# Performance work log

Measured on AMD Instinct MI355X. Metric: run time of the kernel, lower is better.

The kernel has to match this reference:

```python
import jax, jax.numpy as jnp
import numpy as np

N_NODES = 50000
N_EDGES = 600000
N_GRAPHS = 64
IN_DIM = 6
HID = 128


def setup_inputs() -> dict:
    key = jax.random.key(0)
    ks = jax.random.split(key, 10)
    x = jax.random.normal(ks[0], (N_NODES, IN_DIM), dtype=jnp.float32)
    edge_index = jax.random.randint(ks[1], (2, N_EDGES), 0, N_NODES, dtype=jnp.int64)
    batch = jnp.sort(jax.random.randint(ks[2], (N_NODES,), 0, N_GRAPHS, dtype=jnp.int64))
    def glorot(k, shape):
        lim = float(np.sqrt(6.0 / (shape[0] + shape[1])))
        return jax.random.uniform(k, shape, jnp.float32, -lim, lim)
    return {
        'x': x, 'edge_index': edge_index, 'batch': batch,
        'W1': glorot(ks[3], (IN_DIM, HID)), 'b1': jnp.zeros((HID,), jnp.float32),
        'W2': glorot(ks[4], (HID, HID)), 'b2': jnp.zeros((HID,), jnp.float32),
        'W3': glorot(ks[5], (HID, HID)), 'b3': jnp.zeros((HID,), jnp.float32),
        'fc1_w': glorot(ks[6], (HID, 64)), 'fc1_b': jnp.zeros((64,), jnp.float32),
        'fc2_w': glorot(ks[7], (64, 1)), 'fc2_b': jnp.zeros((1,), jnp.float32),
    }


def _gcn_norm(edge_index, n):
    # PyG GCNConv default: add self-loops, symmetric D^-1/2 A D^-1/2 normalization.
    loop = jnp.arange(n, dtype=edge_index.dtype)
    src = jnp.concatenate([edge_index[0], loop])
    dst = jnp.concatenate([edge_index[1], loop])
    deg = jax.ops.segment_sum(jnp.ones_like(dst, dtype=jnp.float32), dst, num_segments=n)
    dis = jnp.where(deg > 0, jax.lax.rsqrt(jnp.maximum(deg, 1.0)), 0.0)
    norm = dis[src] * dis[dst]  # [E+N]
    return src, dst, norm


def _gcn_layer(x, W, b, src, dst, norm, n):
    h = x @ W                       # [N, H] small GEMM
    msg = h[src] * norm[:, None]    # [E+N, H] irregular gather
    out = jax.ops.segment_sum(msg, dst, num_segments=n)  # scatter-add
    return out + b


def reference(x, edge_index, batch, W1, b1, W2, b2, W3, b3, fc1_w, fc1_b, fc2_w, fc2_b):
    n = x.shape[0]
    src, dst, norm = _gcn_norm(edge_index, n)
    h = jax.nn.relu(_gcn_layer(x, W1, b1, src, dst, norm, n))
    h = jax.nn.relu(_gcn_layer(h, W2, b2, src, dst, norm, n))
    h = jax.nn.relu(_gcn_layer(h, W3, b3, src, dst, norm, n))
    # global mean pool over graphs
    sums = jax.ops.segment_sum(h, batch, num_segments=N_GRAPHS)  # [B, H]
    cnt = jax.ops.segment_sum(jnp.ones((n,), jnp.float32), batch, num_segments=N_GRAPHS)
    pooled = sums / jnp.maximum(cnt, 1.0)[:, None]
    z = jax.nn.relu(pooled @ fc1_w + fc1_b)
    return z @ fc2_w + fc2_b  # [B, 1]
```

## Files before the change

### kernel.cpp

```cpp
#include <hip/hip_runtime.h>
#include <hip/hip_fp16.h>

#define HID 128
#define NGRAPH 64
#define CAP 64
#define NPB 16

typedef unsigned int uint32;
typedef unsigned short ushort;
using short8 = __attribute__((ext_vector_type(8))) short;
using f32x4  = __attribute__((ext_vector_type(4))) float;

__device__ __forceinline__ float2 h2f2(uint32 u) {
    __half2 h = *(__half2*)&u;
    return __half22float2(h);
}
__device__ __forceinline__ uint32 f2h2(float a, float b) {
    __half2 h;
    h.x = __float2half(a);
    h.y = __float2half(b);
    return *(uint32*)&h;
}

__device__ __forceinline__ void accum4(float* acc, uint4 v) {
    float2 e0 = h2f2(v.x), e1 = h2f2(v.y), e2 = h2f2(v.z), e3 = h2f2(v.w);
    acc[0] += e0.x; acc[1] += e0.y; acc[2] += e1.x; acc[3] += e1.y;
    acc[4] += e2.x; acc[5] += e2.y; acc[6] += e3.x; acc[7] += e3.y;
}

template<bool F8> struct RowVec;
template<> struct RowVec<false> { uint4 v; };
template<> struct RowVec<true>  { uint2 v; };

template<bool F8>
__device__ __forceinline__ RowVec<F8> ldrow(const uint32* __restrict__ S, int s, int q) {
    RowVec<F8> r;
    if constexpr (F8) r.v = *(const uint2*)(S + (size_t)s * 32 + q * 2);
    else              r.v = *(const uint4*)(S + (size_t)s * 64 + q * 4);
    return r;
}
template<bool F8>
__device__ __forceinline__ void acc8(float* a, RowVec<F8> r) {
    if constexpr (F8) {
        auto e0 = __builtin_amdgcn_cvt_pk_f32_fp8(r.v.x, false);
        auto e1 = __builtin_amdgcn_cvt_pk_f32_fp8(r.v.x, true);
        auto e2 = __builtin_amdgcn_cvt_pk_f32_fp8(r.v.y, false);
        auto e3 = __builtin_amdgcn_cvt_pk_f32_fp8(r.v.y, true);
        a[0] += e0[0]; a[1] += e0[1]; a[2] += e1[0]; a[3] += e1[1];
        a[4] += e2[0]; a[5] += e2[1]; a[6] += e3[0]; a[7] += e3[1];
    } else {
        accum4(a, r.v);
    }
}

__global__ void setup(int* __restrict__ fill, uint32* __restrict__ s1,
                      uint32* __restrict__ s2, const int* __restrict__ batch,
                      int* __restrict__ gstart, float* __restrict__ pooled, int n) {
    int i = blockIdx.x * blockDim.x + threadIdx.x;
    if (i < n) fill[i] = 0;
    if (i < 32) s1[(size_t)n * 32 + i] = 0u;
    if (i < 64) s2[(size_t)n * 64 + i] = 0u;
    if (i < NGRAPH * HID) pooled[i] = 0.f;
    if (i < n) {
        int b0 = batch[i];
        if (i == 0) {
            for (int g = 0; g <= b0; ++g) gstart[g] = 0;
        }
        if (i + 1 < n) {
            int b1 = batch[i + 1];
            for (int g = b0 + 1; g <= b1; ++g) gstart[g] = i + 1;
        } else {
            for (int g = b0 + 1; g <= NGRAPH; ++g) gstart[g] = n;
        }
    }
}

__global__ void csr_fill_pack(const int* __restrict__ src, const int* __restrict__ dst,
                              int* __restrict__ fill, int* __restrict__ csr,
                              int E, int EB4,
                              const float* __restrict__ W2, const float* __restrict__ W3,
                              ushort* __restrict__ wt) {
    int b = blockIdx.x;
    if (b < EB4) {
        int e0 = (b * blockDim.x + threadIdx.x) * 4;
        if (e0 >= E) return;
        if (e0 + 3 < E) {
            int4 d4 = *(const int4*)(dst + e0);
            int4 s4 = *(const int4*)(src + e0);
            int p0 = atomicAdd(&fill[d4.x], 1);
            int p1 = atomicAdd(&fill[d4.y], 1);
            int p2 = atomicAdd(&fill[d4.z], 1);
            int p3 = atomicAdd(&fill[d4.w], 1);
            if (p0 < CAP) csr[(size_t)d4.x * CAP + p0] = s4.x;
            if (p1 < CAP) csr[(size_t)d4.y * CAP + p1] = s4.y;
            if (p2 < CAP) csr[(size_t)d4.z * CAP + p2] = s4.z;
            if (p3 < CAP) csr[(size_t)d4.w * CAP + p3] = s4.w;
        } else {
            for (int e = e0; e < E; ++e) {
                int d = dst[e];
                int pos = atomicAdd(&fill[d], 1);
                if (pos < CAP) csr[(size_t)d * CAP + pos] = src[e];
            }
        }
    } else {
        int t = (b - EB4) * blockDim.x + threadIdx.x;
        int sel = t >> 14;
        int idx = t & 16383;
        int nn = idx >> 7, kk = idx & 127;
        const float* W = sel ? W3 : W2;
        wt[sel * 16384 + idx] = __half_as_ushort(__float2half(W[kk * HID + nn]));
    }
}

__global__ void finalize(const int* __restrict__ fill, float* __restrict__ dis,
                         const float* __restrict__ x, float4* __restrict__ xp4, int n) {
    int i = blockIdx.x * blockDim.x + threadIdx.x;
    if (i >= n) return;
    int d = fill[i] + 1;
    float di = (float)(1.0 / sqrt((double)d));
    dis[i] = di;
    const float* xi = x + (size_t)i * 6;
    xp4[(size_t)i * 2]     = make_float4(di * xi[0], di * xi[1], di * xi[2], di * xi[3]);
    xp4[(size_t)i * 2 + 1] = make_float4(di * xi[4], di * xi[5], 0.f, 0.f);
}

__global__ __launch_bounds__(256) void layer1_quad(
    const float4* __restrict__ xp4, const int* __restrict__ fill,
    const int* __restrict__ csr, const float* __restrict__ dis,
    const float* __restrict__ W1, const float* __restrict__ b1,
    uint32* __restrict__ S1, int n) {
    int t = blockIdx.x * blockDim.x + threadIdx.x;
    int wv = t >> 6;
    int lane = t & 63;
    int sub = lane >> 4;
    int sl  = lane & 15;
    int i = wv * 4 + sub;
    if (i >= n) return;

    int m = fill[i]; if (m > CAP) m = CAP;
    float a0 = 0.f, a1 = 0.f, a2 = 0.f, a3 = 0.f, a4 = 0.f, a5 = 0.f;
#pragma unroll
    for (int r = 0; r < 4; ++r) {
        int slot = sl + 16 * r;
        if (slot < m) {
            int s = csr[(size_t)i * CAP + slot];
            float4 p0 = xp4[(size_t)s * 2];
            float4 p1 = xp4[(size_t)s * 2 + 1];
            a0 += p0.x; a1 += p0.y; a2 += p0.z;
            a3 += p0.w; a4 += p1.x; a5 += p1.y;
        }
    }
#pragma unroll
    for (int off = 8; off > 0; off >>= 1) {
        a0 += __shfl_xor(a0, off); a1 += __shfl_xor(a1, off);
        a2 += __shfl_xor(a2, off); a3 += __shfl_xor(a3, off);
        a4 += __shfl_xor(a4, off); a5 += __shfl_xor(a5, off);
    }
    float di = dis[i];
    float4 s0 = xp4[(size_t)i * 2];
    float4 s1v = xp4[(size_t)i * 2 + 1];
    float xa[6];
    xa[0] = di * (s0.x + a0); xa[1] = di * (s0.y + a1);
    xa[2] = di * (s0.z + a2); xa[3] = di * (s0.w + a3);
    xa[4] = di * (s1v.x + a4); xa[5] = di * (s1v.y + a5);

    int c0 = sl * 8;
    float z[8];
#pragma unroll
    for (int j = 0; j < 8; ++j) z[j] = b1[c0 + j];
#pragma unroll
    for (int k = 0; k < 6; ++k) {
#pragma unroll
        for (int j = 0; j < 8; ++j) z[j] += xa[k] * W1[k * HID + c0 + j];
    }
    float o[8];
#pragma unroll
    for (int j = 0; j < 8; ++j) o[j] = di * fmaxf(z[j], 0.f);
    uint32 r0 = 0, r1 = 0;
    r0 = __builtin_amdgcn_cvt_pk_fp8_f32(o[0], o[1], r0, false);
    r0 = __builtin_amdgcn_cvt_pk_fp8_f32(o[2], o[3], r0, true);
    r1 = __builtin_amdgcn_cvt_pk_fp8_f32(o[4], o[5], r1, false);
    r1 = __builtin_amdgcn_cvt_pk_fp8_f32(o[6], o[7], r1, true);
    *(uint2*)(S1 + (size_t)i * 32 + sl * 2) = make_uint2(r0, r1);
}

template<int MINW, bool F8IN>
__global__ __launch_bounds__(256, MINW) void layer_agg_gemm(
    const uint32* __restrict__ Sin, const int* __restrict__ fill,
    const int* __restrict__ csr, const float* __restrict__ dis,
    const ushort* __restrict__ WT, const float* __restrict__ bias,
    uint32* __restrict__ Sout, int n, int scaleOut) {
    __shared__ uint4 plds4[NPB * 17];
    const int wave = threadIdx.x >> 6;
    const int lane = threadIdx.x & 63;
    const int grp = lane >> 4;
    const int q   = lane & 15;
    const int blk0 = blockIdx.x * NPB;
    const int base = blk0 + wave * 4;

    int mt4[4];
    int idx4[4];
#pragma unroll
    for (int j = 0; j < 4; ++j) {
        int i = base + j;
        int fv = (i < n) ? fill[i] : 0;
        int m = fv > CAP ? CAP : fv;
        idx4[j] = (lane < m) ? csr[(size_t)i * CAP + lane]
                             : ((lane == m && i < n && m < CAP) ? i : n);
        mt4[j] = m + (m < CAP ? 1 : 0);
    }

#pragma unroll
    for (int jp = 0; jp < 2; ++jp) {
        const int ja = jp * 2, jb = ja + 1;
        float acca[8] = {0.f, 0.f, 0.f, 0.f, 0.f, 0.f, 0.f, 0.f};
        float accb[8] = {0.f, 0.f, 0.f, 0.f, 0.f, 0.f, 0.f, 0.f};
        {
            int sa1 = __shfl(idx4[ja], grp);
            int sa2 = __shfl(idx4[ja], 4 + grp);
            int sa3 = __shfl(idx4[ja], 8 + grp);
            int sa4 = __shfl(idx4[ja], 12 + grp);
            int sb1 = __shfl(idx4[jb], grp);
            int sb2 = __shfl(idx4[jb], 4 + grp);
            int sb3 = __shfl(idx4[jb], 8 + grp);
            int sb4 = __shfl(idx4[jb], 12 + grp);
            RowVec<F8IN> va1 = ldrow<F8IN>(Sin, sa1, q);
            RowVec<F8IN> va2 = ldrow<F8IN>(Sin, sa2, q);
            RowVec<F8IN> va3 = ldrow<F8IN>(Sin, sa3, q);
            RowVec<F8IN> va4 = ldrow<F8IN>(Sin, sa4, q);
            RowVec<F8IN> vb1 = ldrow<F8IN>(Sin, sb1, q);
            RowVec<F8IN> vb2 = ldrow<F8IN>(Sin, sb2, q);
            RowVec<F8IN> vb3 = ldrow<F8IN>(Sin, sb3, q);
            RowVec<F8IN> vb4 = ldrow<F8IN>(Sin, sb4, q);
            acc8<F8IN>(acca, va1); acc8<F8IN>(acca, va2);
            acc8<F8IN>(acca, va3); acc8<F8IN>(acca, va4);
            acc8<F8IN>(accb, vb1); acc8<F8IN>(accb, vb2);
            acc8<F8IN>(accb, vb3); acc8<F8IN>(accb, vb4);
        }
        for (int k = 16; k < mt4[ja]; k += 16) {
            int s1 = __shfl(idx4[ja], k + grp);
            int s2 = __shfl(idx4[ja], k + 4 + grp);
            int s3 = __shfl(idx4[ja], k + 8 + grp);
            int s4 = __shfl(idx4[ja], k + 12 + grp);
            RowVec<F8IN> v1 = ldrow<F8IN>(Sin, s1, q);
            RowVec<F8IN> v2 = ldrow<F8IN>(Sin, s2, q);
            RowVec<F8IN> v3 = ldrow<F8IN>(Sin, s3, q);
            RowVec<F8IN> v4 = ldrow<F8IN>(Sin, s4, q);
            acc8<F8IN>(acca, v1); acc8<F8IN>(acca, v2);
            acc8<F8IN>(acca, v3); acc8<F8IN>(acca, v4);
        }
        for (int k = 16; k < mt4[jb]; k += 16) {
            int s1 = __shfl(idx4[jb], k + grp);
            int s2 = __shfl(idx4[jb], k + 4 + grp);
            int s3 = __shfl(idx4[jb], k + 8 + grp);
            int s4 = __shfl(idx4[jb], k + 12 + grp);
            RowVec<F8IN> v1 = ldrow<F8IN>(Sin, s1, q);
            RowVec<F8IN> v2 = ldrow<F8IN>(Sin, s2, q);
            RowVec<F8IN> v3 = ldrow<F8IN>(Sin, s3, q);
            RowVec<F8IN> v4 = ldrow<F8IN>(Sin, s4, q);
            acc8<F8IN>(accb, v1); acc8<F8IN>(accb, v2);
            acc8<F8IN>(accb, v3); acc8<F8IN>(accb, v4);
        }
#pragma unroll
        for (int r = 0; r < 8; ++r) {
            acca[r] += __shfl_xor(acca[r], 16);
            acca[r] += __shfl_xor(acca[r], 32);
            accb[r] += __shfl_xor(accb[r], 16);
            accb[r] += __shfl_xor(accb[r], 32);
        }
        if (grp == 0) {
            int ia = base + ja, ib = base + jb;
            float da = (ia < n) ? dis[ia] : 0.f;
            float db = (ib < n) ? dis[ib] : 0.f;
            plds4[(wave * 4 + ja) * 17 + q] =
                make_uint4(f2h2(da * acca[0], da * acca[1]),
                           f2h2(da * acca[2], da * acca[3]),
                           f2h2(da * acca[4], da * acca[5]),
                           f2h2(da * acca[6], da * acca[7]));
            plds4[(wave * 4 + jb) * 17 + q] =
                make_uint4(f2h2(db * accb[0], db * accb[1]),
                           f2h2(db * accb[2], db * accb[3]),
                           f2h2(db * accb[4], db * accb[5]),
                           f2h2(db * accb[6], db * accb[7]));
        }
    }
    __syncthreads();

    const int l16 = lane & 15, quad = lane >> 4;
    f32x4 acc2[2] = {};
#pragma unroll
    for (int kc = 0; kc < 4; ++kc) {
        int ko = kc * 32 + quad * 8;
        short8 a0 = *(const short8*)&plds4[(size_t)l16 * 17 + kc * 4 + quad];
#pragma unroll
        for (int ct = 0; ct < 2; ++ct) {
            short8 wh = *(const short8*)(WT + (size_t)(wave * 32 + ct * 16 + l16) * HID + ko);
            acc2[ct] = __builtin_amdgcn_mfma_f32_16x16x32_f16(wh, a0, acc2[ct], 0, 0, 0);
        }
    }
    ushort* so = (ushort*)Sout;
    int node = blk0 + l16;
    if (node < n) {
        float sc = scaleOut ? dis[node] : 1.f;
#pragma unroll
        for (int ct = 0; ct < 2; ++ct) {
            int cb = wave * 32 + ct * 16 + quad * 4;
            float4 bv = *(const float4*)(bias + cb);
            float o0 = fmaxf(acc2[ct][0] + bv.x, 0.f) * sc;
            float o1 = fmaxf(acc2[ct][1] + bv.y, 0.f) * sc;
            float o2 = fmaxf(acc2[ct][2] + bv.z, 0.f) * sc;
            float o3 = fmaxf(acc2[ct][3] + bv.w, 0.f) * sc;
            *(uint2*)(so + (size_t)node * HID + cb) = make_uint2(f2h2(o0, o1), f2h2(o2, o3));
        }
    }
}

__global__ __launch_bounds__(256) void pool_partial(
    const uint32* __restrict__ h, const int* __restrict__ gstart,
    float* __restrict__ pooled, int n) {
    __shared__ float red[4][128];
    const int g = blockIdx.x >> 3;
    const int c = blockIdx.x & 7;
    const int t = threadIdx.x;
    const int sub = t >> 6, cc = t & 63;

    const int start = gstart[g], end = gstart[g + 1];
    const int len = end - start;
    const int s0 = start + (int)(((long)len * c) >> 3);
    const int s1 = start + (int)(((long)len * (c + 1)) >> 3);

    float sx = 0.f, sy = 0.f;
    int i = s0 + sub;
    for (; i + 12 < s1; i += 16) {
        uint32 u0 = h[(size_t)i * 64 + cc];
        uint32 u1 = h[(size_t)(i + 4) * 64 + cc];
        uint32 u2 = h[(size_t)(i + 8) * 64 + cc];
        uint32 u3 = h[(size_t)(i + 12) * 64 + cc];
        float2 v0 = h2f2(u0), v1 = h2f2(u1), v2 = h2f2(u2), v3 = h2f2(u3);
        sx += v0.x + v1.x + v2.x + v3.x;
        sy += v0.y + v1.y + v2.y + v3.y;
    }
    for (; i < s1; i += 4) {
        float2 v = h2f2(h[(size_t)i * 64 + cc]);
        sx += v.x; sy += v.y;
    }
    *(float2*)&red[sub][2 * cc] = make_float2(sx, sy);
    __syncthreads();

    if (t < 128) {
        float v = red[0][t] + red[1][t] + red[2][t] + red[3][t];
        atomicAdd(&pooled[g * HID + t], v);
    }
}

__global__ void mlp_head(const float* __restrict__ pooled, const int* __restrict__ gstart,
                         const float* __restrict__ fc1w, const float* __restrict__ fc1b,
                         const float* __restrict__ fc2w, const float* __restrict__ fc2b,
                         float* __restrict__ out) {
    int g = blockIdx.x;
    int j = threadIdx.x;
    float inv = 1.0f / fmaxf((float)(gstart[g + 1] - gstart[g]), 1.0f);
    float z = fc1b[j];
#pragma unroll 8
    for (int k = 0; k < HID; ++k) z += (pooled[g * HID + k] * inv) * fc1w[k * 64 + j];
    z = fmaxf(z, 0.f);
    float v = z * fc2w[j];
#pragma unroll
    for (int off = 32; off > 0; off >>= 1) v += __shfl_down(v, off);
    if (j == 0) out[g] = v + fc2b[0];
}

extern "C" void kernel_launch(void* const* d_in, const int* in_sizes, int n_in,
                              void* d_out, int out_size, void* d_ws, size_t ws_size,
                              hipStream_t stream) {
    const float* x     = (const float*)d_in[0];
    const int*   ei    = (const int*)d_in[1];
    const int*   batch = (const int*)d_in[2];
    const float* W1    = (const float*)d_in[3];
    const float* b1    = (const float*)d_in[4];
    const float* W2    = (const float*)d_in[5];
    const float* b2    = (const float*)d_in[6];
    const float* W3    = (const float*)d_in[7];
    const float* b3    = (const float*)d_in[8];
    const float* fc1w  = (const float*)d_in[9];
    const float* fc1b  = (const float*)d_in[10];
    const float* fc2w  = (const float*)d_in[11];
    const float* fc2b  = (const float*)d_in[12];
    float* out = (float*)d_out;

    const int N = in_sizes[0] / 6;
    const int E = in_sizes[1] / 2;
    const int* src = ei;
    const int* dst = ei + E;

    char* ws = (char*)d_ws;
    char* p = ws;
    uint32* S1   = (uint32*)p;   p += (size_t)(N + 1) * 128;
    uint32* S2   = (uint32*)p;   p += (size_t)(N + 1) * 256;
    uint32* B1h  = (uint32*)p;   p += (size_t)N * 256;
    float4* xp4  = (float4*)p;   p += (size_t)N * 32;
    ushort* WT   = (ushort*)p;   p += 2 * 32768;
    float* dis     = (float*)p;  p += (size_t)N * 4;
    int*   fill    = (int*)p;    p += (size_t)N * 4;
    int*   csr     = (int*)p;    p += (size_t)N * CAP * 4;
    int*   gstart  = (int*)p;    p += (NGRAPH + 1) * 4;
    float* pooled  = (float*)p;  p += NGRAPH * HID * 4;

    const int B = 256;
    const int EB4 = (E + B * 4 - 1) / (B * 4);

    setup<<<(N + B - 1) / B, B, 0, stream>>>(fill, S1, S2, batch, gstart, pooled, N);
    csr_fill_pack<<<EB4 + 128, B, 0, stream>>>(src, dst, fill, csr, E, EB4, W2, W3, WT);
    finalize<<<(N + B - 1) / B, B, 0, stream>>>(fill, dis, x, xp4, N);

    int l1Blocks = (int)(((size_t)N * 16 + B - 1) / B);
    int fusedBlocks = (N + NPB - 1) / NPB;

    layer1_quad<<<l1Blocks, B, 0, stream>>>(xp4, fill, csr, dis, W1, b1, S1, N);

    layer_agg_gemm<6, true><<<fusedBlocks, B, 0, stream>>>(S1, fill, csr, dis, WT, b2, S2, N, 1);

    layer_agg_gemm<5, false><<<fusedBlocks, B, 0, stream>>>(S2, fill, csr, dis, WT + 16384, b3, B1h, N, 0);

    pool_partial<<<NGRAPH * 8, B, 0, stream>>>(B1h, gstart, pooled, N);

    mlp_head<<<NGRAPH, 64, 0, stream>>>(pooled, gstart, fc1w, fc1b, fc2w, fc2b, out);
}
```

Before: 205.0 us.

## Fuse global mean-pool reduction into final GCN layer epilogue

The last aggregation+GEMM layer now reduces its ReLU outputs per graph directly. It stages the 16-node tile in shared memory and atomically adds run-length segment sums into the pooled buffer, using the sorted batch ids. This removes the fp16 write of the final hidden features, the separate pool_partial kernel and its re-read of that buffer. In exchange it adds extra shared memory (which may reduce occupancy for MINW=5), two more barriers, and roughly 128 atomics per block across about 3125 blocks, all contending on 64 graph rows.

```diff
diff --git a/kernel.cpp b/kernel.cpp
--- a/kernel.cpp
+++ b/kernel.cpp
@@ -184,19 +184,30 @@
     *(uint2*)(S1 + (size_t)i * 32 + sl * 2) = make_uint2(r0, r1);
 }
 
-template<int MINW, bool F8IN>
+template<int MINW, bool F8IN, bool POOL>
 __global__ __launch_bounds__(256, MINW) void layer_agg_gemm(
     const uint32* __restrict__ Sin, const int* __restrict__ fill,
     const int* __restrict__ csr, const float* __restrict__ dis,
     const ushort* __restrict__ WT, const float* __restrict__ bias,
-    uint32* __restrict__ Sout, int n, int scaleOut) {
+    uint32* __restrict__ Sout, const int* __restrict__ batch,
+    float* __restrict__ pooled, int n, int scaleOut) {
     __shared__ uint4 plds4[NPB * 17];
+    __shared__ float outp[NPB * 132];
+    __shared__ int   bLds[NPB];
     const int wave = threadIdx.x >> 6;
     const int lane = threadIdx.x & 63;
     const int grp = lane >> 4;
     const int q   = lane & 15;
     const int blk0 = blockIdx.x * NPB;
     const int base = blk0 + wave * 4;
+
+    if constexpr (POOL) {
+        if (threadIdx.x < NPB) {
+            int node = blk0 + threadIdx.x;
+            bLds[threadIdx.x] = (node < n) ? batch[node] : -1;
+        }
+        for (int idx = threadIdx.x; idx < NPB * 132; idx += 256) outp[idx] = 0.f;
+    }
 
     int mt4[4];
     int idx4[4];
@@ -298,58 +309,50 @@
             acc2[ct] = __builtin_amdgcn_mfma_f32_16x16x32_f16(wh, a0, acc2[ct], 0, 0, 0);
         }
     }
-    ushort* so = (ushort*)Sout;
     int node = blk0 + l16;
-    if (node < n) {
-        float sc = scaleOut ? dis[node] : 1.f;
-#pragma unroll
-        for (int ct = 0; ct < 2; ++ct) {
-            int cb = wave * 32 + ct * 16 + quad * 4;
-            float4 bv = *(const float4*)(bias + cb);
-            float o0 = fmaxf(acc2[ct][0] + bv.x, 0.f) * sc;
-            float o1 = fmaxf(acc2[ct][1] + bv.y, 0.f) * sc;
-            float o2 = fmaxf(acc2[ct][2] + bv.z, 0.f) * sc;
-            float o3 = fmaxf(acc2[ct][3] + bv.w, 0.f) * sc;
-            *(uint2*)(so + (size_t)node * HID + cb) = make_uint2(f2h2(o0, o1), f2h2(o2, o3));
-        }
-    }
-}
-
-__global__ __launch_bounds__(256) void pool_partial(
-    const uint32* __restrict__ h, const int* __restrict__ gstart,
-    float* __restrict__ pooled, int n) {
-    __shared__ float red[4][128];
-    const int g = blockIdx.x >> 3;
-    const int c = blockIdx.x & 7;
-    const int t = threadIdx.x;
-    const int sub = t >> 6, cc = t & 63;
-
-    const int start = gstart[g], end = gstart[g + 1];
-    const int len = end - start;
-    const int s0 = start + (int)(((long)len * c) >> 3);
-    const int s1 = start + (int)(((long)len * (c + 1)) >> 3);
-
-    float sx = 0.f, sy = 0.f;
-    int i = s0 + sub;
-    for (; i + 12 < s1; i += 16) {
-        uint32 u0 = h[(size_t)i * 64 + cc];
-        uint32 u1 = h[(size_t)(i + 4) * 64 + cc];
-        uint32 u2 = h[(size_t)(i + 8) * 64 + cc];
-        uint32 u3 = h[(size_t)(i + 12) * 64 + cc];
-        float2 v0 = h2f2(u0), v1 = h2f2(u1), v2 = h2f2(u2), v3 = h2f2(u3);
-        sx += v0.x + v1.x + v2.x + v3.x;
-        sy += v0.y + v1.y + v2.y + v3.y;
-    }
-    for (; i < s1; i += 4) {
-        float2 v = h2f2(h[(size_t)i * 64 + cc]);
-        sx += v.x; sy += v.y;
-    }
-    *(float2*)&red[sub][2 * cc] = make_float2(sx, sy);
-    __syncthreads();
-
-    if (t < 128) {
-        float v = red[0][t] + red[1][t] + red[2][t] + red[3][t];
-        atomicAdd(&pooled[g * HID + t], v);
+    if constexpr (POOL) {
+        __syncthreads();
+        if (node < n) {
+#pragma unroll
+            for (int ct = 0; ct < 2; ++ct) {
+                int cb = wave * 32 + ct * 16 + quad * 4;
+                float4 bv = *(const float4*)(bias + cb);
+                *(float4*)&outp[l16 * 132 + cb] = make_float4(
+                    fmaxf(acc2[ct][0] + bv.x, 0.f), fmaxf(acc2[ct][1] + bv.y, 0.f),
+                    fmaxf(acc2[ct][2] + bv.z, 0.f), fmaxf(acc2[ct][3] + bv.w, 0.f));
+            }
+        }
+        __syncthreads();
+        int t = threadIdx.x;
+        if (t < HID) {
+            float s = 0.f;
+            int curg = bLds[0];
+#pragma unroll
+            for (int r = 0; r < NPB; ++r) {
+                int g = bLds[r];
+                if (g != curg) {
+                    if (curg >= 0) atomicAdd(&pooled[curg * HID + t], s);
+                    s = 0.f; curg = g;
+                }
+                s += outp[r * 132 + t];
+            }
+            if (curg >= 0) atomicAdd(&pooled[curg * HID + t], s);
+        }
+    } else {
+        ushort* so = (ushort*)Sout;
+        if (node < n) {
+            float sc = scaleOut ? dis[node] : 1.f;
+#pragma unroll
+            for (int ct = 0; ct < 2; ++ct) {
+                int cb = wave * 32 + ct * 16 + quad * 4;
+                float4 bv = *(const float4*)(bias + cb);
+                float o0 = fmaxf(acc2[ct][0] + bv.x, 0.f) * sc;
+                float o1 = fmaxf(acc2[ct][1] + bv.y, 0.f) * sc;
+                float o2 = fmaxf(acc2[ct][2] + bv.z, 0.f) * sc;
+                float o3 = fmaxf(acc2[ct][3] + bv.w, 0.f) * sc;
+                *(uint2*)(so + (size_t)node * HID + cb) = make_uint2(f2h2(o0, o1), f2h2(o2, o3));
+            }
+        }
     }
 }
 
@@ -397,7 +400,6 @@
     char* p = ws;
     uint32* S1   = (uint32*)p;   p += (size_t)(N + 1) * 128;
     uint32* S2   = (uint32*)p;   p += (size_t)(N + 1) * 256;
-    uint32* B1h  = (uint32*)p;   p += (size_t)N * 256;
     float4* xp4  = (float4*)p;   p += (size_t)N * 32;
     ushort* WT   = (ushort*)p;   p += 2 * 32768;
     float* dis     = (float*)p;  p += (size_t)N * 4;
@@ -418,11 +420,11 @@
 
     layer1_quad<<<l1Blocks, B, 0, stream>>>(xp4, fill, csr, dis, W1, b1, S1, N);
 
-    layer_agg_gemm<6, true><<<fusedBlocks, B, 0, stream>>>(S1, fill, csr, dis, WT, b2, S2, N, 1);
-
-    layer_agg_gemm<5, false><<<fusedBlocks, B, 0, stream>>>(S2, fill, csr, dis, WT + 16384, b3, B1h, N, 0);
-
-    pool_partial<<<NGRAPH * 8, B, 0, stream>>>(B1h, gstart, pooled, N);
+    layer_agg_gemm<6, true, false><<<fusedBlocks, B, 0, stream>>>(
+        S1, fill, csr, dis, WT, b2, S2, nullptr, nullptr, N, 1);
+
+    layer_agg_gemm<5, false, true><<<fusedBlocks, B, 0, stream>>>(
+        S2, fill, csr, dis, WT + 16384, b3, nullptr, batch, pooled, N, 0);
 
     mlp_head<<<NGRAPH, 64, 0, stream>>>(pooled, gstart, fc1w, fc1b, fc2w, fc2b, out);
 }
```

After: 198.9 us. -3.0%, faster.
